# Performance work log

Measured on AMD Instinct MI355X. Metric: run time of the kernel, lower is better.

The kernel has to match this reference:

```python
import jax, jax.numpy as jnp
import numpy as np

B, S, H, N, D = 2, 2048, 1024, 16, 64  # batch, seq, hidden, heads, head_size
PAD = -30000.0


def setup_inputs() -> dict:
    key = jax.random.key(0)
    kx, kqkv, kout, krpe = jax.random.split(key, 4)
    x = jax.random.normal(kx, (B, S, H), jnp.float32)
    qkv = jax.random.normal(kqkv, (H, 3, N, D), jnp.float32) * H ** (-0.5)
    out_w = jax.random.normal(kout, (N, D, H), jnp.float32) * (N * D) ** (-0.5)
    # rpe_bias is zero-init in torch; use small randn so the bias path is exercised
    rpe_bias = jax.random.normal(krpe, (N, S), jnp.float32) * 0.02
    return {"x": x, "qkv": qkv, "out_w": out_w, "rpe_bias": rpe_bias}


def reference(x, qkv, out_w, rpe_bias):
    # q, k, v: [B, N, S, D]
    q, k, v = jnp.einsum('bsx,xMnd->Mbnsd', x, qkv)
    s = x.shape[1]
    a = jnp.einsum('bnsd,bntd->bnst', q, k) * q.shape[-1] ** (-0.5)
    # cumulative relative-position bias: bias[n, i, j] = cumsum(rpe)[n, i-j] for i>=j,
    # PAD otherwise (exactly what to_tril produces on the row-broadcast cumsum).
    cum = jnp.cumsum(rpe_bias[:, :s], axis=-1)            # [N, S]
    rel = jnp.arange(s)[:, None] - jnp.arange(s)[None, :]  # [S, S], i - j
    bias = jnp.where(rel >= 0, cum[:, jnp.clip(rel, 0)], PAD)  # [N, S, S]
    a = jax.nn.softmax(a + bias, axis=-1)
    mix = jnp.einsum('bnst,bntd->bnsd', a, v)
    return jnp.einsum('bnsd,ndx->bsx', mix, out_w)
```

## Files before the change

### kernel.cpp

```cpp
#include <hip/hip_runtime.h>
#include <hip/hip_bf16.h>
#include <cstdint>
#include <cstddef>

#define B_   2
#define S_   2048
#define H_   1024
#define NH   16
#define DH   64
#define LOG2E 1.4426950408889634f
#define SCALE2 (0.125f * LOG2E)

typedef __hip_bfloat16 bf16;
typedef short bf16x8 __attribute__((ext_vector_type(8)));
typedef float f32x4 __attribute__((ext_vector_type(4)));

#define MFMA16(a, b, c) __builtin_amdgcn_mfma_f32_16x16x32_bf16((a), (b), (c), 0, 0, 0)

__device__ __forceinline__ void async16(const void* g, void* l) {
  __builtin_amdgcn_global_load_lds(
      (const __attribute__((address_space(1))) void*)g,
      (__attribute__((address_space(3))) void*)l,
      16, 0, 0);
}
__device__ __forceinline__ void async4(const void* g, void* l) {
  __builtin_amdgcn_global_load_lds(
      (const __attribute__((address_space(1))) void*)g,
      (__attribute__((address_space(3))) void*)l,
      4, 0, 0);
}

__device__ __forceinline__ void tr_body(const float* __restrict__ src,
                                        bf16* __restrict__ dst, int R, int C,
                                        int c0, int r0, bf16 (*tile)[33], int tid) {
  int tx = tid & 31, ty = tid >> 5;
  for (int i = 0; i < 32; i += 8)
    tile[ty + i][tx] = __float2bfloat16(src[(size_t)(r0 + ty + i) * C + c0 + tx]);
  __syncthreads();
  for (int i = 0; i < 32; i += 8)
    dst[(size_t)(c0 + ty + i) * R + r0 + tx] = tile[tx][ty + i];
}

__global__ __launch_bounds__(256)
void prep(const float* __restrict__ x, bf16* __restrict__ xb,
          const float* __restrict__ qkv, bf16* __restrict__ qkvT,
          const float* __restrict__ outw, bf16* __restrict__ outwT,
          const float* __restrict__ rpe, float* __restrict__ cum) {
  __shared__ char pm[2176] __attribute__((aligned(16)));
  const int L = blockIdx.x, tid = threadIdx.x;
  if (L < 4096) {
    int i = (L * 256 + tid) * 4;
    float4 v = *(const float4*)(x + i);
    bf16 o[4] = {__float2bfloat16(v.x), __float2bfloat16(v.y),
                 __float2bfloat16(v.z), __float2bfloat16(v.w)};
    *(uint64_t*)(xb + i) = *(const uint64_t*)o;
  } else if (L < 7168) {
    int t = L - 4096;
    int cx = t % 96, ry = t / 96;
    tr_body(qkv, qkvT, 1024, 3072, cx * 32, ry * 32, (bf16(*)[33])pm, tid);
  } else if (L < 8192) {
    int t = L - 7168;
    int cx = t & 31, ry = t >> 5;
    tr_body(outw, outwT, 1024, 1024, cx * 32, ry * 32, (bf16(*)[33])pm, tid);
  } else {
    float* ssum = (float*)pm;
    int n = L - 8192;
    float loc[8];
    float s = 0.f;
    int base = tid * 8;
#pragma unroll
    for (int u = 0; u < 8; ++u) {
      loc[u] = rpe[n * S_ + base + u];
      s += loc[u];
    }
    ssum[tid] = s;
    __syncthreads();
    float own = s;
    for (int off = 1; off < 256; off <<= 1) {
      float v = (tid >= off) ? ssum[tid - off] : 0.f;
      __syncthreads();
      ssum[tid] += v;
      __syncthreads();
    }
    float run = ssum[tid] - own;
#pragma unroll
    for (int u = 0; u < 8; ++u) {
      run += loc[u];
      cum[n * S_ + base + u] = run * LOG2E;
    }
  }
}

template <int MODE>
__global__ __launch_bounds__(256, MODE == 0 ? 3 : 2)
void gemm_bt(const bf16* __restrict__ A, const bf16* __restrict__ Bt,
             bf16* __restrict__ C0, bf16* __restrict__ C1, bf16* __restrict__ C2,
             float* __restrict__ F0) {
  constexpr int NT = (MODE == 0) ? 4 : 2;
  constexpr int NB = NT * 32;
  __shared__ char smem[MODE == 0 ? 36864 : 12288] __attribute__((aligned(16)));
  bf16* As = (bf16*)smem;
  bf16* Bs = (bf16*)(smem + 8192);
  const int tid = threadIdx.x, lane = tid & 63, w = tid >> 6;
  const int lr = lane & 15, lq = lane >> 4;
  const int m0 = blockIdx.y * 128, n0 = blockIdx.x * NB;
  const int wm = (w & 1) * 64, wn = (w >> 1) * (NT * 16);

  f32x4 acc[4][NT] = {};

  for (int k0 = 0; k0 < 1024; k0 += 32) {
    __syncthreads();
#pragma unroll
    for (int t = 0; t < 2; ++t) {
      int c = (t * 4 + w) * 64 + lane;
      int row = c >> 2, ch = c & 3;
      int k8 = (ch ^ ((row >> 1) & 3)) * 8;
      async16(A + (size_t)(m0 + row) * 1024 + k0 + k8,
              (char*)As + (size_t)(t * 4 + w) * 1024 + lane * 16);
    }
#pragma unroll
    for (int t = 0; t < NB / 64; ++t) {
      int c = (t * 4 + w) * 64 + lane;
      int row = c >> 2, ch = c & 3;
      int k8 = (ch ^ ((row >> 1) & 3)) * 8;
      async16(Bt + (size_t)(n0 + row) * 1024 + k0 + k8,
              (char*)Bs + (size_t)(t * 4 + w) * 1024 + lane * 16);
    }
    __syncthreads();
    bf16x8 af[4], bfr[NT];
#pragma unroll
    for (int mt = 0; mt < 4; ++mt) {
      int row = wm + mt * 16 + lr;
      af[mt] = *(const bf16x8*)(As + row * 32 + ((lq ^ ((row >> 1) & 3)) << 3));
    }
#pragma unroll
    for (int nt = 0; nt < NT; ++nt) {
      int row = wn + nt * 16 + lr;
      bfr[nt] = *(const bf16x8*)(Bs + row * 32 + ((lq ^ ((row >> 1) & 3)) << 3));
    }
#pragma unroll
    for (int mt = 0; mt < 4; ++mt)
#pragma unroll
      for (int nt = 0; nt < NT; ++nt)
        acc[mt][nt] = MFMA16(af[mt], bfr[nt], acc[mt][nt]);
  }

  if (MODE == 0) {
    __syncthreads();
    bf16* E = (bf16*)smem + w * (64 * 72);
    const int cbase = n0 + wn;
    const int mm = cbase >> 10, nn = (cbase >> 6) & 15;
    const int bb = (m0 + wm) >> 11;
    const int sbase = (m0 + wm) & 2047;
    if (mm < 2) {
#pragma unroll
      for (int mt = 0; mt < 4; ++mt)
#pragma unroll
        for (int nt = 0; nt < 4; ++nt)
#pragma unroll
          for (int r = 0; r < 4; ++r)
            E[(mt * 16 + lq * 4 + r) * 72 + nt * 16 + lr] =
                __float2bfloat16(acc[mt][nt][r]);
      bf16* dst = (mm == 0 ? C0 : C1) +
                  ((size_t)(bb * NH + nn) * S_ + sbase) * DH;
#pragma unroll
      for (int it = 0; it < 8; ++it) {
        int c = it * 64 + lane;
        int rw = c >> 3, c8 = c & 7;
        *(uint4*)(dst + (size_t)rw * DH + c8 * 8) =
            *(const uint4*)(E + rw * 72 + c8 * 8);
      }
    } else {
#pragma unroll
      for (int mt = 0; mt < 4; ++mt)
#pragma unroll
        for (int nt = 0; nt < 4; ++nt)
#pragma unroll
          for (int r = 0; r < 4; ++r)
            E[(nt * 16 + lr) * 72 + mt * 16 + lq * 4 + r] =
                __float2bfloat16(acc[mt][nt][r]);
      bf16* dst = C2 + (size_t)(bb * NH + nn) * DH * S_;
#pragma unroll
      for (int it = 0; it < 8; ++it) {
        int c = it * 64 + lane;
        int dr = c >> 3, c8 = c & 7;
        *(uint4*)(dst + (size_t)dr * S_ + sbase + c8 * 8) =
            *(const uint4*)(E + dr * 72 + c8 * 8);
      }
    }
  } else {
#pragma unroll
    for (int mt = 0; mt < 4; ++mt)
#pragma unroll
      for (int nt = 0; nt < NT; ++nt)
#pragma unroll
        for (int r = 0; r < 4; ++r) {
          int rM = m0 + wm + mt * 16 + lq * 4 + r;
          int cN = n0 + wn + nt * 16 + lr;
          F0[(size_t)rM * 1024 + cN] = acc[mt][nt][r];
        }
  }
}

__device__ __forceinline__ void fa_stage(const bf16* __restrict__ k,
                                         const bf16* __restrict__ vt,
                                         const float* __restrict__ cumn,
                                         char* smem, int bn, int i0p, int j0p,
                                         int buf, int lane, int w, int tid) {
  char* dst = smem + buf * 32768;
  const char* ksrc = (const char*)(k + ((size_t)bn * S_ + j0p) * DH);
#pragma unroll
  for (int t = 0; t < 4; ++t) {
    int cb = t * 4 + w;
    int row = cb * 8 + (lane >> 3);
    int cs = (lane & 7) ^ (row & 7);
    async16(ksrc + row * 128 + cs * 16, dst + cb * 1024 + lane * 16);
  }
  const char* vsrc = (const char*)(vt + (size_t)bn * DH * S_);
#pragma unroll
  for (int t = 0; t < 4; ++t) {
    int cb = t * 4 + w;
    int row = cb * 4 + (lane >> 4);
    int cs = (lane & 15) ^ (row & 15);
    async16(vsrc + (size_t)row * (S_ * 2) + j0p * 2 + cs * 16,
            dst + 16384 + cb * 1024 + lane * 16);
  }
  float* cdst = (float*)(smem + 100352) + buf * 1056;
  int base = i0p - j0p - 127 + tid;
#pragma unroll
  for (int p = 0; p < 4; ++p) {
    int src = base + p;
    src = src < 0 ? 0 : (src > S_ - 1 ? S_ - 1 : src);
    async4(cumn + src, cdst + p * 264 + w * 64 + lane);
  }
}

__global__ __launch_bounds__(256, 1)
void fa_kernel(const bf16* __restrict__ q, const bf16* __restrict__ k,
               const bf16* __restrict__ vt, const float* __restrict__ cum,
               bf16* __restrict__ mix) {
  __shared__ char smem[108800] __attribute__((aligned(16)));
  bf16* Ps = (bf16*)(smem + 65536);

  const int tid = threadIdx.x, lane = tid & 63, w = tid >> 6;
  const int lr = lane & 15, lq = lane >> 4;

  const int L = blockIdx.x;
  const int xcd = L & 7, slot = L >> 3;
  const int bn = xcd + 8 * (slot & 3);
  const int pr = slot >> 2;
  const int n = bn & (NH - 1);
  const int b = bn >> 4;
  const float* cumn = cum + n * S_;

  const int T0 = 15 - pr;
  const int T1 = pr;
  const int nj0 = T0 + 1;

  bf16x8 ones;
#pragma unroll
  for (int u = 0; u < 8; ++u) ones[u] = (short)0x3F80;
  const f32x4 fz = {0.f, 0.f, 0.f, 0.f};

  fa_stage(k, vt, cumn, smem, bn, T0 << 7, 0, 0, lane, w, tid);

  f32x4 oacc[2][4];
  f32x4 lacc[2];
  bf16x8 qf[2][2];
  int ti = T0, jt = 0, i0 = T0 << 7;

  for (int g = 0; g < 17; ++g) {
    const int bsel = g & 1;
    const char* kb = smem + bsel * 32768;
    const char* vb = kb + 16384;
    const float* cumB = (const float*)(smem + 100352) + bsel * 1056;
    const bool diag = (jt == ti);

    __syncthreads();

    if (g + 1 < 17) {
      int gn = g + 1, tin, jtn;
      if (gn < nj0) { tin = T0; jtn = gn; }
      else          { tin = T1; jtn = gn - nj0; }
      fa_stage(k, vt, cumn, smem, bn, tin << 7, jtn << 7, bsel ^ 1, lane, w, tid);
    }

    if (jt == 0) {
      const bf16* qbase = q + ((size_t)bn * S_ + i0 + w * 32) * DH;
#pragma unroll
      for (int is = 0; is < 2; ++is)
#pragma unroll
        for (int kt = 0; kt < 2; ++kt)
          qf[is][kt] = *(const bf16x8*)(qbase + (is * 16 + lr) * DH + kt * 32 + lq * 8);
#pragma unroll
      for (int is = 0; is < 2; ++is) {
        lacc[is] = fz;
#pragma unroll
        for (int dt = 0; dt < 4; ++dt) oacc[is][dt] = fz;
      }
    }

    f32x4 sa[2][8] = {};
#pragma unroll
    for (int kt = 0; kt < 2; ++kt)
#pragma unroll
      for (int nt = 0; nt < 8; ++nt) {
        int krow = nt * 16 + lr;
        bf16x8 kf = *(const bf16x8*)(kb + krow * 128 +
                        (((kt * 4 + lq) ^ (krow & 7)) << 4));
        sa[0][nt] = MFMA16(kf, qf[0][kt], sa[0][nt]);
        sa[1][nt] = MFMA16(kf, qf[1][kt], sa[1][nt]);
      }

#pragma unroll
    for (int is = 0; is < 2; ++is) {
      const int ilocI = w * 32 + is * 16 + lr;
      if (!diag) {
#pragma unroll
        for (int nt = 0; nt < 8; ++nt) {
          int jl = nt * 16 + lq * 4;
          int Xm3 = 124 + ilocI - jl;
          int p = Xm3 & 3, b0 = Xm3 & ~3;
          f32x4 cv = *(const f32x4*)(cumB + p * 264 + b0);
          bf16 pk[4];
#pragma unroll
          for (int r = 0; r < 4; ++r)
            pk[r] = __float2bfloat16(exp2f(sa[is][nt][r] * SCALE2 + cv[3 - r]));
          *(uint64_t*)(Ps + ilocI * 136 + nt * 16 + lq * 4) = *(const uint64_t*)pk;
        }
      } else {
#pragma unroll
        for (int nt = 0; nt < 8; ++nt) {
          int jl = nt * 16 + lq * 4;
          int Xm3 = 124 + ilocI - jl;
          int p = Xm3 & 3, b0 = Xm3 & ~3;
          f32x4 cv = *(const f32x4*)(cumB + p * 264 + b0);
          bf16 pk[4];
#pragma unroll
          for (int r = 0; r < 4; ++r) {
            float pv = (ilocI - jl - r >= 0)
                           ? exp2f(sa[is][nt][r] * SCALE2 + cv[3 - r])
                           : 0.f;
            pk[r] = __float2bfloat16(pv);
          }
          *(uint64_t*)(Ps + ilocI * 136 + nt * 16 + lq * 4) = *(const uint64_t*)pk;
        }
      }
    }

#pragma unroll
    for (int kt2 = 0; kt2 < 4; ++kt2) {
      bf16x8 pf0 = *(const bf16x8*)(Ps + (w * 32 + lr) * 136 + kt2 * 32 + lq * 8);
      bf16x8 pf1 = *(const bf16x8*)(Ps + (w * 32 + 16 + lr) * 136 + kt2 * 32 + lq * 8);
      lacc[0] = MFMA16(pf0, ones, lacc[0]);
      lacc[1] = MFMA16(pf1, ones, lacc[1]);
#pragma unroll
      for (int dt = 0; dt < 4; ++dt) {
        int vrow = dt * 16 + lr;
        bf16x8 vf = *(const bf16x8*)(vb + vrow * 256 +
                        (((kt2 * 4 + lq) ^ (vrow & 15)) << 4));
        oacc[0][dt] = MFMA16(pf0, vf, oacc[0][dt]);
        oacc[1][dt] = MFMA16(pf1, vf, oacc[1][dt]);
      }
    }

    if (diag) {
#pragma unroll
      for (int is = 0; is < 2; ++is)
#pragma unroll
        for (int dt = 0; dt < 4; ++dt)
#pragma unroll
          for (int r = 0; r < 4; ++r) {
            int i = i0 + w * 32 + is * 16 + lq * 4 + r;
            int d = dt * 16 + lr;
            mix[((size_t)(b * S_ + i) * NH + n) * DH + d] =
                __float2bfloat16(oacc[is][dt][r] / lacc[is][r]);
          }
      ti = T1; jt = 0; i0 = T1 << 7;
    } else {
      ++jt;
    }
  }
}

extern "C" void kernel_launch(void* const* d_in, const int* in_sizes, int n_in,
                              void* d_out, int out_size, void* d_ws, size_t ws_size,
                              hipStream_t stream) {
  const float* x     = (const float*)d_in[0];
  const float* qkv   = (const float*)d_in[1];
  const float* out_w = (const float*)d_in[2];
  const float* rpe   = (const float*)d_in[3];
  float* out = (float*)d_out;

  char* ws = (char*)d_ws;
  bf16* qkvT  = (bf16*)(ws + 0);
  bf16* outwT = (bf16*)(ws + 6291456);
  bf16* xb    = (bf16*)(ws + 8388608);
  bf16* qb    = (bf16*)(ws + 16777216);
  bf16* kb    = (bf16*)(ws + 25165824);
  bf16* vtb   = (bf16*)(ws + 33554432);
  bf16* mixb  = (bf16*)(ws + 41943040);
  float* cum  = (float*)(ws + 50331648);

  prep<<<8208, 256, 0, stream>>>(x, xb, qkv, qkvT, out_w, outwT, rpe, cum);
  gemm_bt<0><<<dim3(3072 / 128, 4096 / 128), 256, 0, stream>>>(xb, qkvT, qb, kb, vtb, nullptr);
  fa_kernel<<<256, 256, 0, stream>>>(qb, kb, vtb, cum, mixb);
  gemm_bt<1><<<dim3(1024 / 64, 4096 / 128), 256, 0, stream>>>(mixb, outwT, nullptr, nullptr, nullptr, out);
}
```

Measured before the change: 205.6 us.

## Split paired causal tiles into separate blocks with 64-wide KV tiles

The flash-attention kernel no longer processes a balanced pair of 128-row query tiles per block. It launches 512 blocks, each owning one query tile, and walks the KV sequence in 64-column steps. Shared memory drops from about 106KB to 58KB and launch bounds allow two blocks per CU, aiming for more resident waves to hide latency and a finer causal cutoff at the diagonal. In exchange, per-block load becomes imbalanced (2 to 32 iterations), the causal mask now runs on two steps per tile instead of one, and each KV step does less MFMA work per barrier.

Result: faster. 194.0 us (-5.7%).

```diff
diff --git a/kernel.cpp b/kernel.cpp
--- a/kernel.cpp
+++ b/kernel.cpp
@@ -205,106 +205,95 @@
 __device__ __forceinline__ void fa_stage(const bf16* __restrict__ k,
                                          const bf16* __restrict__ vt,
                                          const float* __restrict__ cumn,
-                                         char* smem, int bn, int i0p, int j0p,
-                                         int buf, int lane, int w, int tid) {
-  char* dst = smem + buf * 32768;
-  const char* ksrc = (const char*)(k + ((size_t)bn * S_ + j0p) * DH);
-#pragma unroll
-  for (int t = 0; t < 4; ++t) {
-    int cb = t * 4 + w;
-    int row = cb * 8 + (lane >> 3);
-    int cs = (lane & 7) ^ (row & 7);
-    async16(ksrc + row * 128 + cs * 16, dst + cb * 1024 + lane * 16);
+                                         char* smem, int bn, int i0, int j0,
+                                         int buf, int tid) {
+  char* dst = smem + buf * 16384;
+  const char* ksrc = (const char*)(k + ((size_t)bn * S_ + j0) * DH);
+#pragma unroll
+  for (int t = 0; t < 2; ++t) {
+    int c = t * 256 + tid;
+    int row = c >> 3, ch = c & 7;
+    int cs = ch ^ (row & 7);
+    async16(ksrc + row * 128 + cs * 16, dst + c * 16);
   }
   const char* vsrc = (const char*)(vt + (size_t)bn * DH * S_);
 #pragma unroll
-  for (int t = 0; t < 4; ++t) {
-    int cb = t * 4 + w;
-    int row = cb * 4 + (lane >> 4);
-    int cs = (lane & 15) ^ (row & 15);
-    async16(vsrc + (size_t)row * (S_ * 2) + j0p * 2 + cs * 16,
-            dst + 16384 + cb * 1024 + lane * 16);
-  }
-  float* cdst = (float*)(smem + 100352) + buf * 1056;
-  int base = i0p - j0p - 127 + tid;
+  for (int t = 0; t < 2; ++t) {
+    int c = t * 256 + tid;
+    int row = c >> 3, ch = c & 7;
+    int cs = ch ^ (row & 7);
+    async16(vsrc + (size_t)row * (S_ * 2) + j0 * 2 + cs * 16,
+            dst + 8192 + c * 16);
+  }
+  float* cdst = (float*)(smem + 51200) + buf * 1056;
+  int base = i0 - j0 - 63 + tid;
 #pragma unroll
   for (int p = 0; p < 4; ++p) {
     int src = base + p;
     src = src < 0 ? 0 : (src > S_ - 1 ? S_ - 1 : src);
-    async4(cumn + src, cdst + p * 264 + w * 64 + lane);
-  }
-}
-
-__global__ __launch_bounds__(256, 1)
+    async4(cumn + src, cdst + p * 264 + tid);
+  }
+}
+
+__global__ __launch_bounds__(256, 2)
 void fa_kernel(const bf16* __restrict__ q, const bf16* __restrict__ k,
                const bf16* __restrict__ vt, const float* __restrict__ cum,
                bf16* __restrict__ mix) {
-  __shared__ char smem[108800] __attribute__((aligned(16)));
-  bf16* Ps = (bf16*)(smem + 65536);
+  __shared__ char smem[59648] __attribute__((aligned(16)));
+  bf16* Ps = (bf16*)(smem + 32768);
 
   const int tid = threadIdx.x, lane = tid & 63, w = tid >> 6;
   const int lr = lane & 15, lq = lane >> 4;
 
   const int L = blockIdx.x;
-  const int xcd = L & 7, slot = L >> 3;
+  const int half = L >> 8;
+  const int idx = L & 255;
+  const int xcd = idx & 7, slot = idx >> 3;
   const int bn = xcd + 8 * (slot & 3);
   const int pr = slot >> 2;
+  const int ti = half ? pr : (15 - pr);
   const int n = bn & (NH - 1);
   const int b = bn >> 4;
   const float* cumn = cum + n * S_;
 
-  const int T0 = 15 - pr;
-  const int T1 = pr;
-  const int nj0 = T0 + 1;
+  const int i0 = ti << 7;
+  const int NI = 2 * ti + 2;
+
+  const bf16* qbase = q + ((size_t)bn * S_ + i0 + w * 32) * DH;
+  bf16x8 qf[2][2];
+#pragma unroll
+  for (int is = 0; is < 2; ++is)
+#pragma unroll
+    for (int kt = 0; kt < 2; ++kt)
+      qf[is][kt] = *(const bf16x8*)(qbase + (is * 16 + lr) * DH + kt * 32 + lq * 8);
 
   bf16x8 ones;
 #pragma unroll
   for (int u = 0; u < 8; ++u) ones[u] = (short)0x3F80;
-  const f32x4 fz = {0.f, 0.f, 0.f, 0.f};
-
-  fa_stage(k, vt, cumn, smem, bn, T0 << 7, 0, 0, lane, w, tid);
-
-  f32x4 oacc[2][4];
-  f32x4 lacc[2];
-  bf16x8 qf[2][2];
-  int ti = T0, jt = 0, i0 = T0 << 7;
-
-  for (int g = 0; g < 17; ++g) {
+
+  f32x4 oacc[2][4] = {};
+  f32x4 lacc[2] = {};
+
+  fa_stage(k, vt, cumn, smem, bn, i0, 0, 0, tid);
+
+  for (int g = 0; g < NI; ++g) {
     const int bsel = g & 1;
-    const char* kb = smem + bsel * 32768;
-    const char* vb = kb + 16384;
-    const float* cumB = (const float*)(smem + 100352) + bsel * 1056;
-    const bool diag = (jt == ti);
-
-    __syncthreads();
-
-    if (g + 1 < 17) {
-      int gn = g + 1, tin, jtn;
-      if (gn < nj0) { tin = T0; jtn = gn; }
-      else          { tin = T1; jtn = gn - nj0; }
-      fa_stage(k, vt, cumn, smem, bn, tin << 7, jtn << 7, bsel ^ 1, lane, w, tid);
-    }
-
-    if (jt == 0) {
-      const bf16* qbase = q + ((size_t)bn * S_ + i0 + w * 32) * DH;
-#pragma unroll
-      for (int is = 0; is < 2; ++is)
-#pragma unroll
-        for (int kt = 0; kt < 2; ++kt)
-          qf[is][kt] = *(const bf16x8*)(qbase + (is * 16 + lr) * DH + kt * 32 + lq * 8);
-#pragma unroll
-      for (int is = 0; is < 2; ++is) {
-        lacc[is] = fz;
-#pragma unroll
-        for (int dt = 0; dt < 4; ++dt) oacc[is][dt] = fz;
-      }
-    }
-
-    f32x4 sa[2][8] = {};
+    const char* kb = smem + bsel * 16384;
+    const char* vb = kb + 8192;
+    const float* cumB = (const float*)(smem + 51200) + bsel * 1056;
+    const int j0 = g << 6;
+    const int doff = i0 - j0;
+
+    __syncthreads();
+
+    if (g + 1 < NI)
+      fa_stage(k, vt, cumn, smem, bn, i0, (g + 1) << 6, bsel ^ 1, tid);
+
+    f32x4 sa[2][4] = {};
 #pragma unroll
     for (int kt = 0; kt < 2; ++kt)
 #pragma unroll
-      for (int nt = 0; nt < 8; ++nt) {
+      for (int nt = 0; nt < 4; ++nt) {
         int krow = nt * 16 + lr;
         bf16x8 kf = *(const bf16x8*)(kb + krow * 128 +
                         (((kt * 4 + lq) ^ (krow & 7)) << 4));
@@ -315,72 +304,67 @@
 #pragma unroll
     for (int is = 0; is < 2; ++is) {
       const int ilocI = w * 32 + is * 16 + lr;
-      if (!diag) {
-#pragma unroll
-        for (int nt = 0; nt < 8; ++nt) {
+      if (doff >= 64) {
+#pragma unroll
+        for (int nt = 0; nt < 4; ++nt) {
           int jl = nt * 16 + lq * 4;
-          int Xm3 = 124 + ilocI - jl;
+          int Xm3 = 60 + ilocI - jl;
           int p = Xm3 & 3, b0 = Xm3 & ~3;
           f32x4 cv = *(const f32x4*)(cumB + p * 264 + b0);
           bf16 pk[4];
 #pragma unroll
           for (int r = 0; r < 4; ++r)
             pk[r] = __float2bfloat16(exp2f(sa[is][nt][r] * SCALE2 + cv[3 - r]));
-          *(uint64_t*)(Ps + ilocI * 136 + nt * 16 + lq * 4) = *(const uint64_t*)pk;
+          *(uint64_t*)(Ps + ilocI * 72 + nt * 16 + lq * 4) = *(const uint64_t*)pk;
         }
       } else {
 #pragma unroll
-        for (int nt = 0; nt < 8; ++nt) {
+        for (int nt = 0; nt < 4; ++nt) {
           int jl = nt * 16 + lq * 4;
-          int Xm3 = 124 + ilocI - jl;
+          int Xm3 = 60 + ilocI - jl;
           int p = Xm3 & 3, b0 = Xm3 & ~3;
           f32x4 cv = *(const f32x4*)(cumB + p * 264 + b0);
           bf16 pk[4];
 #pragma unroll
           for (int r = 0; r < 4; ++r) {
-            float pv = (ilocI - jl - r >= 0)
+            float pv = (doff + ilocI - jl - r >= 0)
                            ? exp2f(sa[is][nt][r] * SCALE2 + cv[3 - r])
                            : 0.f;
             pk[r] = __float2bfloat16(pv);
           }
-          *(uint64_t*)(Ps + ilocI * 136 + nt * 16 + lq * 4) = *(const uint64_t*)pk;
+          *(uint64_t*)(Ps + ilocI * 72 + nt * 16 + lq * 4) = *(const uint64_t*)pk;
         }
       }
     }
 
 #pragma unroll
-    for (int kt2 = 0; kt2 < 4; ++kt2) {
-      bf16x8 pf0 = *(const bf16x8*)(Ps + (w * 32 + lr) * 136 + kt2 * 32 + lq * 8);
-      bf16x8 pf1 = *(const bf16x8*)(Ps + (w * 32 + 16 + lr) * 136 + kt2 * 32 + lq * 8);
+    for (int kt2 = 0; kt2 < 2; ++kt2) {
+      bf16x8 pf0 = *(const bf16x8*)(Ps + (w * 32 + lr) * 72 + kt2 * 32 + lq * 8);
+      bf16x8 pf1 = *(const bf16x8*)(Ps + (w * 32 + 16 + lr) * 72 + kt2 * 32 + lq * 8);
       lacc[0] = MFMA16(pf0, ones, lacc[0]);
       lacc[1] = MFMA16(pf1, ones, lacc[1]);
 #pragma unroll
       for (int dt = 0; dt < 4; ++dt) {
         int vrow = dt * 16 + lr;
-        bf16x8 vf = *(const bf16x8*)(vb + vrow * 256 +
-                        (((kt2 * 4 + lq) ^ (vrow & 15)) << 4));
+        bf16x8 vf = *(const bf16x8*)(vb + vrow * 128 +
+                        (((kt2 * 4 + lq) ^ (vrow & 7)) << 4));
         oacc[0][dt] = MFMA16(pf0, vf, oacc[0][dt]);
         oacc[1][dt] = MFMA16(pf1, vf, oacc[1][dt]);
       }
     }
-
-    if (diag) {
-#pragma unroll
-      for (int is = 0; is < 2; ++is)
-#pragma unroll
-        for (int dt = 0; dt < 4; ++dt)
-#pragma unroll
-          for (int r = 0; r < 4; ++r) {
-            int i = i0 + w * 32 + is * 16 + lq * 4 + r;
-            int d = dt * 16 + lr;
-            mix[((size_t)(b * S_ + i) * NH + n) * DH + d] =
-                __float2bfloat16(oacc[is][dt][r] / lacc[is][r]);
-          }
-      ti = T1; jt = 0; i0 = T1 << 7;
-    } else {
-      ++jt;
-    }
-  }
+  }
+
+#pragma unroll
+  for (int is = 0; is < 2; ++is)
+#pragma unroll
+    for (int dt = 0; dt < 4; ++dt)
+#pragma unroll
+      for (int r = 0; r < 4; ++r) {
+        int i = i0 + w * 32 + is * 16 + lq * 4 + r;
+        int d = dt * 16 + lr;
+        mix[((size_t)(b * S_ + i) * NH + n) * DH + d] =
+            __float2bfloat16(oacc[is][dt][r] / lacc[is][r]);
+      }
 }
 
 extern "C" void kernel_launch(void* const* d_in, const int* in_sizes, int n_in,
@@ -404,6 +388,6 @@
 
   prep<<<8208, 256, 0, stream>>>(x, xb, qkv, qkvT, out_w, outwT, rpe, cum);
   gemm_bt<0><<<dim3(3072 / 128, 4096 / 128), 256, 0, stream>>>(xb, qkvT, qb, kb, vtb, nullptr);
-  fa_kernel<<<256, 256, 0, stream>>>(qb, kb, vtb, cum, mixb);
+  fa_kernel<<<512, 256, 0, stream>>>(qb, kb, vtb, cum, mixb);
   gemm_bt<1><<<dim3(1024 / 64, 4096 / 128), 256, 0, stream>>>(mixb, outwT, nullptr, nullptr, nullptr, out);
 }
```
